# Kernel optimization log

Measured on AMD Instinct MI355X. Metric: run time of the kernel, lower is better.

## Reference

```python
import jax, jax.numpy as jnp
import numpy as np

ALPHA = 1.702  # sigmoid-GLU scale
LIMIT = 7.0    # clamp limit
TOP_K = 2      # num_experts_per_tok


def setup_inputs() -> dict:
    key = jax.random.key(0)
    ks = jax.random.split(key, 4)
    B, S, H, E, I = 2, 1024, 1024, 8, 2048
    return {
        "hidden_states": jax.random.normal(ks[0], (B, S, H), jnp.float32),
        "router_weight": jax.random.normal(ks[1], (E, H), jnp.float32),
        "router_bias": jnp.zeros((E,), jnp.float32),
        "gate_up_proj": jax.random.normal(ks[2], (E, H, 2 * I), jnp.float32) * 0.02,
        "gate_up_bias": jnp.zeros((E, 2 * I), jnp.float32),
        "down_proj": jax.random.normal(ks[3], (E, I, H), jnp.float32) * 0.02,
        "down_bias": jnp.zeros((E, H), jnp.float32),
    }


def reference(hidden_states, router_weight, router_bias, gate_up_proj,
              gate_up_bias, down_proj, down_bias):
    B, S, H = hidden_states.shape
    E, _, two_I = gate_up_proj.shape
    I = two_I // 2

    flat = hidden_states.reshape(B * S, H)  # [T, H]

    # Router: softmax + top-k
    logits = flat @ router_weight.T + router_bias            # [T, E]
    scores = jax.nn.softmax(logits, axis=-1)
    topk_w, topk_idx = jax.lax.top_k(scores, TOP_K)          # [T, K]

    # Dense per-expert gated FFN (einsum 'abmh,ehn->abemn' computes all experts
    # on all tokens; the reshape/permute dance is a mathematical no-op).
    gu = jnp.einsum('th,ehn->ten', flat, gate_up_proj) + gate_up_bias  # [T, E, 2I]
    gate = jnp.minimum(gu[..., :I], LIMIT)
    up = jnp.clip(gu[..., I:], -LIMIT, LIMIT)
    glu = gate * jax.nn.sigmoid(gate * ALPHA)
    act = (up + 1.0) * glu                                   # [T, E, I]

    down = jnp.einsum('tei,eih->teh', act, down_proj) + down_bias  # [T, E, H]

    # Combine: gather each token's top-k expert outputs, weighted sum.
    gathered = jnp.take_along_axis(down, topk_idx[:, :, None], axis=1)  # [T, K, H]
    out = (gathered * topk_w[:, :, None]).sum(axis=1)        # [T, H]
    return out.reshape(B, S, H)
```

## Files before the change

### kernel.cpp

```cpp
#include <hip/hip_runtime.h>
#include <math.h>

#define TT 2048
#define HH 1024
#define EE 8
#define II 2048
#define N1 4096
#define ALPHA 1.702f
#define LIMIT 7.0f

typedef __attribute__((ext_vector_type(8))) short short8;
typedef __attribute__((ext_vector_type(4))) float floatx4;
typedef __attribute__((ext_vector_type(4))) unsigned int uintx4;

__device__ __forceinline__ short f2bf(float f) {
  union { float f; unsigned u; } v; v.f = f;
  unsigned r = (v.u + 0x7fffu + ((v.u >> 16) & 1u)) >> 16;
  return (short)r;
}
__device__ __forceinline__ unsigned cvt2(float lo, float hi) {
  unsigned r;
  asm("v_cvt_pk_bf16_f32 %0, %1, %2" : "=v"(r) : "v"(lo), "v"(hi));
  return r;
}
__device__ __forceinline__ void gload16(const void* g, void* l) {
  __builtin_amdgcn_global_load_lds(
      (const __attribute__((address_space(1))) unsigned int*)g,
      (__attribute__((address_space(3))) unsigned int*)l, 16, 0, 0);
}

__global__ __launch_bounds__(256) void convert_x(const float* __restrict__ x,
                                                 unsigned short* __restrict__ xb) {
  const int id = blockIdx.x * 256 + threadIdx.x;
  const float4 a = ((const float4*)x)[id * 2];
  const float4 b = ((const float4*)x)[id * 2 + 1];
  uintx4 w;
  w[0] = cvt2(a.x, a.y); w[1] = cvt2(a.z, a.w);
  w[2] = cvt2(b.x, b.y); w[3] = cvt2(b.z, b.w);
  ((uintx4*)xb)[id] = w;
}

__global__ __launch_bounds__(256) void transpose_bf16(
    const float* __restrict__ src, unsigned short* __restrict__ dst,
    const int K, const int N) {
  const int e = blockIdx.z;
  const int n0 = blockIdx.x * 64, k0 = blockIdx.y * 64;
  __shared__ float tile[64][68];
  const float* s = src + (size_t)e * K * N;
  unsigned short* d = dst + (size_t)e * N * K;
  const int t = threadIdx.x;
  const int nq = t & 15, kr = t >> 4;
#pragma unroll
  for (int r = 0; r < 4; r++) {
    const int k = r * 16 + kr;
    const float4 v = *(const float4*)(s + (size_t)(k0 + k) * N + n0 + nq * 4);
    tile[k][nq * 4 + 0] = v.x; tile[k][nq * 4 + 1] = v.y;
    tile[k][nq * 4 + 2] = v.z; tile[k][nq * 4 + 3] = v.w;
  }
  __syncthreads();
  const int n = t >> 2, ks = (t & 3) * 16;
  unsigned short* orow = d + (size_t)(n0 + n) * K + k0 + ks;
  uintx4 w0, w1;
#pragma unroll
  for (int m = 0; m < 4; m++)
    w0[m] = cvt2(tile[ks + 2 * m][n], tile[ks + 2 * m + 1][n]);
#pragma unroll
  for (int m = 0; m < 4; m++)
    w1[m] = cvt2(tile[ks + 8 + 2 * m][n], tile[ks + 9 + 2 * m][n]);
  *(uintx4*)orow = w0;
  *(uintx4*)(orow + 8) = w1;
}

__global__ __launch_bounds__(256) void router_kernel(
    const float* __restrict__ x, const float* __restrict__ rw,
    const float* __restrict__ rb, int* __restrict__ topk_idx,
    float* __restrict__ topk_w) {
  const int t = blockIdx.x;
  const float* xr = x + (size_t)t * HH;
  const int lane = threadIdx.x & 63;
  const int wave = threadIdx.x >> 6;
  float xv[16];
#pragma unroll
  for (int i = 0; i < 16; i++) xv[i] = xr[lane + i * 64];
  __shared__ float logits[EE];
#pragma unroll
  for (int ee = 0; ee < 2; ee++) {
    const int e = wave * 2 + ee;
    const float* wr = rw + (size_t)e * HH;
    float s = 0.f;
#pragma unroll
    for (int i = 0; i < 16; i++) s += xv[i] * wr[lane + i * 64];
#pragma unroll
    for (int off = 32; off > 0; off >>= 1) s += __shfl_down(s, off, 64);
    if (lane == 0) logits[e] = s + rb[e];
  }
  __syncthreads();
  if (threadIdx.x == 0) {
    float l[EE], sc[EE];
    float mx = -3.4e38f;
    for (int i = 0; i < EE; i++) { l[i] = logits[i]; mx = fmaxf(mx, l[i]); }
    float sum = 0.f;
    for (int i = 0; i < EE; i++) { sc[i] = expf(l[i] - mx); sum += sc[i]; }
    const float inv = 1.f / sum;
    int i0 = 0;
    for (int i = 1; i < EE; i++) if (sc[i] > sc[i0]) i0 = i;
    int i1 = (i0 == 0) ? 1 : 0;
    for (int i = 0; i < EE; i++) if (i != i0 && sc[i] > sc[i1]) i1 = i;
    topk_idx[t * 2 + 0] = i0;
    topk_idx[t * 2 + 1] = i1;
    topk_w[t * 2 + 0] = sc[i0] * inv;
    topk_w[t * 2 + 1] = sc[i1] * inv;
  }
}

__global__ void assign_kernel(const int* __restrict__ topk_idx,
                              int* __restrict__ counts, int* __restrict__ rows) {
  const int id = blockIdx.x * blockDim.x + threadIdx.x;
  if (id >= TT * 2) return;
  const int e = topk_idx[id];
  const int slot = atomicAdd(&counts[e], 1);
  rows[e * TT + slot] = id;
}

__global__ __launch_bounds__(256, 4) void gemm_gu(
    const unsigned short* __restrict__ xb, const unsigned short* __restrict__ gupt,
    const float* __restrict__ gub, const int* __restrict__ counts,
    const int* __restrict__ rows, unsigned short* __restrict__ act) {
  const int e = blockIdx.z, mtile = blockIdx.y, ntile = blockIdx.x;
  const int count = counts[e];
  if (mtile * 128 >= count) return;
  const int* rl = rows + e * TT + mtile * 128;
  __shared__ __align__(16) char smem[33280];
  unsigned short* As = (unsigned short*)smem;
  unsigned short* Bs = (unsigned short*)(smem + 16384);
  float* glds = (float*)smem;
  const int tid = threadIdx.x;
  const int lane = tid & 63, wave = tid >> 6;
  const int wm = (wave & 1) << 6, wn = (wave >> 1) << 6;
  const int quad = lane >> 4, r16 = lane & 15;

  const int lrow = lane >> 2, lko = (lane & 3) * 8;
  const int q0 = wave * 2, q1 = q0 + 1;
  const int row0 = q0 * 16 + lrow, row1 = q1 * 16 + lrow;
  const int last = count - 1 - mtile * 128;
  const int cr0 = row0 <= last ? row0 : last;
  const int cr1 = row1 <= last ? row1 : last;
  const unsigned short* pA0 = xb + (size_t)(rl[cr0] >> 1) * HH + lko;
  const unsigned short* pA1 = xb + (size_t)(rl[cr1] >> 1) * HH + lko;
  const int bn0 = (row0 < 64) ? (ntile * 64 + row0) : (II + ntile * 64 + row0 - 64);
  const int bn1 = (row1 < 64) ? (ntile * 64 + row1) : (II + ntile * 64 + row1 - 64);
  const unsigned short* pB0 = gupt + (size_t)e * N1 * HH + (size_t)bn0 * HH + lko;
  const unsigned short* pB1 = gupt + (size_t)e * N1 * HH + (size_t)bn1 * HH + lko;
  unsigned short* dA0 = As + q0 * 512;
  unsigned short* dA1 = As + q1 * 512;
  unsigned short* dB0 = Bs + q0 * 512;
  unsigned short* dB1 = Bs + q1 * 512;

  floatx4 acc[4][4] = {};
  const int NTK = HH / 32;

#define STAGE(B, kk) do { \
    const int ko_ = (kk) * 32; \
    gload16(pA0 + ko_, dA0 + (B) * 4096); \
    gload16(pA1 + ko_, dA1 + (B) * 4096); \
    gload16(pB0 + ko_, dB0 + (B) * 4096); \
    gload16(pB1 + ko_, dB1 + (B) * 4096); \
  } while (0)

#define PHASE(B) do { \
    asm volatile("s_waitcnt vmcnt(4)" ::: "memory"); \
    __builtin_amdgcn_s_barrier(); \
    short8 af[4], bf4[4]; \
    _Pragma("unroll") for (int i = 0; i < 4; i++) \
      af[i] = *(const short8*)(As + (B) * 4096 + (wm + i * 16 + r16) * 32 + quad * 8); \
    _Pragma("unroll") for (int j = 0; j < 4; j++) \
      bf4[j] = *(const short8*)(Bs + (B) * 4096 + (wn + j * 16 + r16) * 32 + quad * 8); \
    asm volatile("s_waitcnt lgkmcnt(0)" ::: "memory"); \
    __builtin_amdgcn_sched_barrier(0); \
    __builtin_amdgcn_s_barrier(); \
    { const int ks_ = kn < NTK ? kn : NTK - 1; kn++; STAGE(B, ks_); } \
    __builtin_amdgcn_sched_barrier(0); \
    __builtin_amdgcn_s_setprio(1); \
    _Pragma("unroll") for (int i = 0; i < 4; i++) \
      _Pragma("unroll") for (int j = 0; j < 4; j++) \
        acc[i][j] = __builtin_amdgcn_mfma_f32_16x16x32_bf16(af[i], bf4[j], acc[i][j], 0, 0, 0); \
    __builtin_amdgcn_s_setprio(0); \
  } while (0)

  STAGE(0, 0);
  STAGE(1, 1);
  int kn = 2;
#pragma unroll 1
  for (int t = 0; t < NTK; t += 2) {
    PHASE(0);
    PHASE(1);
  }
  asm volatile("s_waitcnt vmcnt(0)" ::: "memory");
  __builtin_amdgcn_s_barrier();

  const int colbase = ntile * 64;
  if (wn == 0) {
#pragma unroll
    for (int j = 0; j < 4; j++) {
      const int c = j * 16 + r16;
      const float gb = gub[e * N1 + colbase + c];
#pragma unroll
      for (int i = 0; i < 4; i++)
#pragma unroll
        for (int reg = 0; reg < 4; reg++) {
          const int rr = wm + i * 16 + quad * 4 + reg;
          float g = acc[i][j][reg] + gb;
          g = fminf(g, LIMIT);
          glds[rr * 65 + c] = g / (1.f + expf(-g * ALPHA));
        }
    }
  }
  __builtin_amdgcn_s_barrier();
  if (wn == 64) {
#pragma unroll
    for (int j = 0; j < 4; j++) {
      const int c = j * 16 + r16;
      const float ub = gub[e * N1 + II + colbase + c];
#pragma unroll
      for (int i = 0; i < 4; i++)
#pragma unroll
        for (int reg = 0; reg < 4; reg++) {
          const int rr = wm + i * 16 + quad * 4 + reg;
          if (mtile * 128 + rr < count) {
            float u = acc[i][j][reg] + ub;
            u = fminf(fmaxf(u, -LIMIT), LIMIT);
            const float glu = glds[rr * 65 + c];
            act[(size_t)rl[rr] * II + colbase + c] = (unsigned short)f2bf((u + 1.f) * glu);
          }
        }
    }
  }
#undef STAGE
#undef PHASE
}

__global__ __launch_bounds__(256, 4) void gemm_down(
    const unsigned short* __restrict__ act, const unsigned short* __restrict__ dpt,
    const float* __restrict__ db, const int* __restrict__ counts,
    const int* __restrict__ rows, float* __restrict__ dout) {
  const int e = blockIdx.z >> 2, kc = blockIdx.z & 3;
  const int mtile = blockIdx.y, ntile = blockIdx.x;
  const int count = counts[e];
  if (mtile * 128 >= count) return;
  const int kb = kc * (II / 4);
  const int* rl = rows + e * TT + mtile * 128;
  __shared__ __align__(16) char smem[32768];
  unsigned short* As = (unsigned short*)smem;
  unsigned short* Bs = (unsigned short*)(smem + 16384);
  const int tid = threadIdx.x;
  const int lane = tid & 63, wave = tid >> 6;
  const int wm = (wave & 1) << 6, wn = (wave >> 1) << 6;
  const int quad = lane >> 4, r16 = lane & 15;

  const int lrow = lane >> 2, lko = (lane & 3) * 8;
  const int q0 = wave * 2, q1 = q0 + 1;
  const int row0 = q0 * 16 + lrow, row1 = q1 * 16 + lrow;
  const int last = count - 1 - mtile * 128;
  const int cr0 = row0 <= last ? row0 : last;
  const int cr1 = row1 <= last ? row1 : last;
  const unsigned short* pA0 = act + (size_t)rl[cr0] * II + kb + lko;
  const unsigned short* pA1 = act + (size_t)rl[cr1] * II + kb + lko;
  const unsigned short* pB0 = dpt + (size_t)e * HH * II + (size_t)(ntile * 128 + row0) * II + kb + lko;
  const unsigned short* pB1 = dpt + (size_t)e * HH * II + (size_t)(ntile * 128 + row1) * II + kb + lko;
  unsigned short* dA0 = As + q0 * 512;
  unsigned short* dA1 = As + q1 * 512;
  unsigned short* dB0 = Bs + q0 * 512;
  unsigned short* dB1 = Bs + q1 * 512;

  floatx4 acc[4][4] = {};
  const int NTK = (II / 4) / 32;

#define STAGE(B, kk) do { \
    const int ko_ = (kk) * 32; \
    gload16(pA0 + ko_, dA0 + (B) * 4096); \
    gload16(pA1 + ko_, dA1 + (B) * 4096); \
    gload16(pB0 + ko_, dB0 + (B) * 4096); \
    gload16(pB1 + ko_, dB1 + (B) * 4096); \
  } while (0)

#define PHASE(B) do { \
    asm volatile("s_waitcnt vmcnt(4)" ::: "memory"); \
    __builtin_amdgcn_s_barrier(); \
    short8 af[4], bf4[4]; \
    _Pragma("unroll") for (int i = 0; i < 4; i++) \
      af[i] = *(const short8*)(As + (B) * 4096 + (wm + i * 16 + r16) * 32 + quad * 8); \
    _Pragma("unroll") for (int j = 0; j < 4; j++) \
      bf4[j] = *(const short8*)(Bs + (B) * 4096 + (wn + j * 16 + r16) * 32 + quad * 8); \
    asm volatile("s_waitcnt lgkmcnt(0)" ::: "memory"); \
    __builtin_amdgcn_sched_barrier(0); \
    __builtin_amdgcn_s_barrier(); \
    { const int ks_ = kn < NTK ? kn : NTK - 1; kn++; STAGE(B, ks_); } \
    __builtin_amdgcn_sched_barrier(0); \
    __builtin_amdgcn_s_setprio(1); \
    _Pragma("unroll") for (int i = 0; i < 4; i++) \
      _Pragma("unroll") for (int j = 0; j < 4; j++) \
        acc[i][j] = __builtin_amdgcn_mfma_f32_16x16x32_bf16(af[i], bf4[j], acc[i][j], 0, 0, 0); \
    __builtin_amdgcn_s_setprio(0); \
  } while (0)

  STAGE(0, 0);
  STAGE(1, 1);
  int kn = 2;
#pragma unroll 1
  for (int t = 0; t < NTK; t += 2) {
    PHASE(0);
    PHASE(1);
  }
  asm volatile("s_waitcnt vmcnt(0)" ::: "memory");
  __builtin_amdgcn_s_barrier();

  float* dc = dout + (size_t)kc * ((size_t)TT * 2 * HH);
#pragma unroll
  for (int i = 0; i < 4; i++) {
#pragma unroll
    for (int reg = 0; reg < 4; reg++) {
      const int rr = wm + i * 16 + quad * 4 + reg;
      if (mtile * 128 + rr < count) {
        const int ent = rl[rr];
        float* orow = dc + (size_t)ent * HH + ntile * 128;
#pragma unroll
        for (int j = 0; j < 4; j++) {
          const int c = wn + j * 16 + r16;
          float v = acc[i][j][reg];
          if (kc == 0) v += db[e * HH + ntile * 128 + c];
          orow[c] = v;
        }
      }
    }
  }
#undef STAGE
#undef PHASE
}

__global__ void combine_kernel(const float* __restrict__ dout,
                               const float* __restrict__ tw,
                               float* __restrict__ out) {
  const int id = blockIdx.x * blockDim.x + threadIdx.x;
  const int t = id >> 8;
  const int h = (id & 255) * 4;
  const float w0 = tw[t * 2], w1 = tw[t * 2 + 1];
  const size_t CH = (size_t)TT * 2 * HH;
  const size_t r0 = (size_t)(2 * t) * HH + h;
  const size_t r1 = (size_t)(2 * t + 1) * HH + h;
  float4 a = {0.f, 0.f, 0.f, 0.f}, b = {0.f, 0.f, 0.f, 0.f};
#pragma unroll
  for (int c = 0; c < 4; c++) {
    const float4 va = *(const float4*)(dout + c * CH + r0);
    const float4 vb = *(const float4*)(dout + c * CH + r1);
    a.x += va.x; a.y += va.y; a.z += va.z; a.w += va.w;
    b.x += vb.x; b.y += vb.y; b.z += vb.z; b.w += vb.w;
  }
  float4 o;
  o.x = w0 * a.x + w1 * b.x;
  o.y = w0 * a.y + w1 * b.y;
  o.z = w0 * a.z + w1 * b.z;
  o.w = w0 * a.w + w1 * b.w;
  *(float4*)(out + (size_t)t * HH + h) = o;
}

extern "C" void kernel_launch(void* const* d_in, const int* in_sizes, int n_in,
                              void* d_out, int out_size, void* d_ws, size_t ws_size,
                              hipStream_t stream) {
  const float* x   = (const float*)d_in[0];
  const float* rw  = (const float*)d_in[1];
  const float* rb  = (const float*)d_in[2];
  const float* gup = (const float*)d_in[3];
  const float* gub = (const float*)d_in[4];
  const float* dp  = (const float*)d_in[5];
  const float* db  = (const float*)d_in[6];
  float* out = (float*)d_out;

  char* ws = (char*)d_ws;
  int*   topk_idx = (int*)(ws + 0);
  float* topk_w   = (float*)(ws + 16384);
  int*   counts   = (int*)(ws + 32768);
  int*   rows     = (int*)(ws + 33024);
  unsigned short* xb   = (unsigned short*)(ws + 131072);
  unsigned short* gupt = (unsigned short*)(ws + 4325376);
  unsigned short* dpt  = (unsigned short*)(ws + 71434240);
  unsigned short* act  = (unsigned short*)(ws + 104988672);
  float* dout = (float*)(ws + 4325376);

  convert_x<<<TT * HH / 8 / 256, 256, 0, stream>>>(x, xb);
  transpose_bf16<<<dim3(N1 / 64, HH / 64, EE), 256, 0, stream>>>(gup, gupt, HH, N1);
  transpose_bf16<<<dim3(HH / 64, II / 64, EE), 256, 0, stream>>>(dp, dpt, II, HH);
  router_kernel<<<TT, 256, 0, stream>>>(x, rw, rb, topk_idx, topk_w);
  hipMemsetAsync(counts, 0, 64, stream);
  assign_kernel<<<(TT * 2 + 255) / 256, 256, 0, stream>>>(topk_idx, counts, rows);
  gemm_gu<<<dim3(II / 64, TT / 128, EE), 256, 0, stream>>>(xb, gupt, gub, counts, rows, act);
  gemm_down<<<dim3(HH / 128, TT / 128, EE * 4), 256, 0, stream>>>(act, dpt, db, counts, rows, dout);
  combine_kernel<<<(TT * HH / 4) / 256, 256, 0, stream>>>(dout, topk_w, out);
}
```

Measured before the change: 429.1 us.

## Fuse router with bf16 conversion and assignment, combine via atomics, deepen pipeline

Folds the x-to-bf16 conversion and the expert-slot assignment into the router kernel, which removes two launches. The combine kernel and the partial-sum buffer go away: the down GEMM now scales by the top-k weight and atomically adds into a zeroed output, with the K split cut from 4 to 2. Both GEMMs move from a 2-stage to a 4-stage LDS pipeline with 64KB shared memory and launch bounds lowered to 2 blocks. The trade-offs are fewer resident blocks per CU, float atomic contention on the output, and a nondeterministic order of accumulation.

```diff
diff --git a/kernel.cpp b/kernel.cpp
--- a/kernel.cpp
+++ b/kernel.cpp
@@ -27,17 +27,6 @@
   __builtin_amdgcn_global_load_lds(
       (const __attribute__((address_space(1))) unsigned int*)g,
       (__attribute__((address_space(3))) unsigned int*)l, 16, 0, 0);
-}
-
-__global__ __launch_bounds__(256) void convert_x(const float* __restrict__ x,
-                                                 unsigned short* __restrict__ xb) {
-  const int id = blockIdx.x * 256 + threadIdx.x;
-  const float4 a = ((const float4*)x)[id * 2];
-  const float4 b = ((const float4*)x)[id * 2 + 1];
-  uintx4 w;
-  w[0] = cvt2(a.x, a.y); w[1] = cvt2(a.z, a.w);
-  w[2] = cvt2(b.x, b.y); w[3] = cvt2(b.z, b.w);
-  ((uintx4*)xb)[id] = w;
 }
 
 __global__ __launch_bounds__(256) void transpose_bf16(
@@ -73,8 +62,9 @@
 
 __global__ __launch_bounds__(256) void router_kernel(
     const float* __restrict__ x, const float* __restrict__ rw,
-    const float* __restrict__ rb, int* __restrict__ topk_idx,
-    float* __restrict__ topk_w) {
+    const float* __restrict__ rb, float* __restrict__ topk_w,
+    int* __restrict__ counts, int* __restrict__ rows,
+    unsigned short* __restrict__ xb) {
   const int t = blockIdx.x;
   const float* xr = x + (size_t)t * HH;
   const int lane = threadIdx.x & 63;
@@ -93,6 +83,11 @@
 #pragma unroll
     for (int off = 32; off > 0; off >>= 1) s += __shfl_down(s, off, 64);
     if (lane == 0) logits[e] = s + rb[e];
+  }
+  if (wave == 0) {
+    unsigned short* xo = xb + (size_t)t * HH;
+#pragma unroll
+    for (int i = 0; i < 16; i++) xo[lane + i * 64] = (unsigned short)f2bf(xv[i]);
   }
   __syncthreads();
   if (threadIdx.x == 0) {
@@ -106,23 +101,16 @@
     for (int i = 1; i < EE; i++) if (sc[i] > sc[i0]) i0 = i;
     int i1 = (i0 == 0) ? 1 : 0;
     for (int i = 0; i < EE; i++) if (i != i0 && sc[i] > sc[i1]) i1 = i;
-    topk_idx[t * 2 + 0] = i0;
-    topk_idx[t * 2 + 1] = i1;
     topk_w[t * 2 + 0] = sc[i0] * inv;
     topk_w[t * 2 + 1] = sc[i1] * inv;
-  }
-}
-
-__global__ void assign_kernel(const int* __restrict__ topk_idx,
-                              int* __restrict__ counts, int* __restrict__ rows) {
-  const int id = blockIdx.x * blockDim.x + threadIdx.x;
-  if (id >= TT * 2) return;
-  const int e = topk_idx[id];
-  const int slot = atomicAdd(&counts[e], 1);
-  rows[e * TT + slot] = id;
-}
-
-__global__ __launch_bounds__(256, 4) void gemm_gu(
+    const int s0 = atomicAdd(&counts[i0], 1);
+    rows[i0 * TT + s0] = t * 2 + 0;
+    const int s1 = atomicAdd(&counts[i1], 1);
+    rows[i1 * TT + s1] = t * 2 + 1;
+  }
+}
+
+__global__ __launch_bounds__(256, 2) void gemm_gu(
     const unsigned short* __restrict__ xb, const unsigned short* __restrict__ gupt,
     const float* __restrict__ gub, const int* __restrict__ counts,
     const int* __restrict__ rows, unsigned short* __restrict__ act) {
@@ -130,9 +118,9 @@
   const int count = counts[e];
   if (mtile * 128 >= count) return;
   const int* rl = rows + e * TT + mtile * 128;
-  __shared__ __align__(16) char smem[33280];
+  __shared__ __align__(16) char smem[65536];
   unsigned short* As = (unsigned short*)smem;
-  unsigned short* Bs = (unsigned short*)(smem + 16384);
+  unsigned short* Bs = (unsigned short*)(smem + 32768);
   float* glds = (float*)smem;
   const int tid = threadIdx.x;
   const int lane = tid & 63, wave = tid >> 6;
@@ -168,7 +156,7 @@
   } while (0)
 
 #define PHASE(B) do { \
-    asm volatile("s_waitcnt vmcnt(4)" ::: "memory"); \
+    asm volatile("s_waitcnt vmcnt(12)" ::: "memory"); \
     __builtin_amdgcn_s_barrier(); \
     short8 af[4], bf4[4]; \
     _Pragma("unroll") for (int i = 0; i < 4; i++) \
@@ -189,11 +177,15 @@
 
   STAGE(0, 0);
   STAGE(1, 1);
-  int kn = 2;
+  STAGE(2, 2);
+  STAGE(3, 3);
+  int kn = 4;
 #pragma unroll 1
-  for (int t = 0; t < NTK; t += 2) {
+  for (int t = 0; t < NTK; t += 4) {
     PHASE(0);
     PHASE(1);
+    PHASE(2);
+    PHASE(3);
   }
   asm volatile("s_waitcnt vmcnt(0)" ::: "memory");
   __builtin_amdgcn_s_barrier();
@@ -239,19 +231,20 @@
 #undef PHASE
 }
 
-__global__ __launch_bounds__(256, 4) void gemm_down(
+__global__ __launch_bounds__(256, 2) void gemm_down(
     const unsigned short* __restrict__ act, const unsigned short* __restrict__ dpt,
     const float* __restrict__ db, const int* __restrict__ counts,
-    const int* __restrict__ rows, float* __restrict__ dout) {
-  const int e = blockIdx.z >> 2, kc = blockIdx.z & 3;
+    const int* __restrict__ rows, const float* __restrict__ tw,
+    float* __restrict__ out) {
+  const int e = blockIdx.z >> 1, kc = blockIdx.z & 1;
   const int mtile = blockIdx.y, ntile = blockIdx.x;
   const int count = counts[e];
   if (mtile * 128 >= count) return;
-  const int kb = kc * (II / 4);
+  const int kb = kc * (II / 2);
   const int* rl = rows + e * TT + mtile * 128;
-  __shared__ __align__(16) char smem[32768];
+  __shared__ __align__(16) char smem[65536];
   unsigned short* As = (unsigned short*)smem;
-  unsigned short* Bs = (unsigned short*)(smem + 16384);
+  unsigned short* Bs = (unsigned short*)(smem + 32768);
   const int tid = threadIdx.x;
   const int lane = tid & 63, wave = tid >> 6;
   const int wm = (wave & 1) << 6, wn = (wave >> 1) << 6;
@@ -273,7 +266,7 @@
   unsigned short* dB1 = Bs + q1 * 512;
 
   floatx4 acc[4][4] = {};
-  const int NTK = (II / 4) / 32;
+  const int NTK = (II / 2) / 32;
 
 #define STAGE(B, kk) do { \
     const int ko_ = (kk) * 32; \
@@ -284,7 +277,7 @@
   } while (0)
 
 #define PHASE(B) do { \
-    asm volatile("s_waitcnt vmcnt(4)" ::: "memory"); \
+    asm volatile("s_waitcnt vmcnt(12)" ::: "memory"); \
     __builtin_amdgcn_s_barrier(); \
     short8 af[4], bf4[4]; \
     _Pragma("unroll") for (int i = 0; i < 4; i++) \
@@ -305,16 +298,19 @@
 
   STAGE(0, 0);
   STAGE(1, 1);
-  int kn = 2;
+  STAGE(2, 2);
+  STAGE(3, 3);
+  int kn = 4;
 #pragma unroll 1
-  for (int t = 0; t < NTK; t += 2) {
+  for (int t = 0; t < NTK; t += 4) {
     PHASE(0);
     PHASE(1);
+    PHASE(2);
+    PHASE(3);
   }
   asm volatile("s_waitcnt vmcnt(0)" ::: "memory");
   __builtin_amdgcn_s_barrier();
 
-  float* dc = dout + (size_t)kc * ((size_t)TT * 2 * HH);
 #pragma unroll
   for (int i = 0; i < 4; i++) {
 #pragma unroll
@@ -322,45 +318,20 @@
       const int rr = wm + i * 16 + quad * 4 + reg;
       if (mtile * 128 + rr < count) {
         const int ent = rl[rr];
-        float* orow = dc + (size_t)ent * HH + ntile * 128;
+        const float w = tw[ent];
+        float* orow = out + (size_t)(ent >> 1) * HH + ntile * 128;
 #pragma unroll
         for (int j = 0; j < 4; j++) {
           const int c = wn + j * 16 + r16;
           float v = acc[i][j][reg];
           if (kc == 0) v += db[e * HH + ntile * 128 + c];
-          orow[c] = v;
+          atomicAdd(&orow[c], w * v);
         }
       }
     }
   }
 #undef STAGE
 #undef PHASE
-}
-
-__global__ void combine_kernel(const float* __restrict__ dout,
-                               const float* __restrict__ tw,
-                               float* __restrict__ out) {
-  const int id = blockIdx.x * blockDim.x + threadIdx.x;
-  const int t = id >> 8;
-  const int h = (id & 255) * 4;
-  const float w0 = tw[t * 2], w1 = tw[t * 2 + 1];
-  const size_t CH = (size_t)TT * 2 * HH;
-  const size_t r0 = (size_t)(2 * t) * HH + h;
-  const size_t r1 = (size_t)(2 * t + 1) * HH + h;
-  float4 a = {0.f, 0.f, 0.f, 0.f}, b = {0.f, 0.f, 0.f, 0.f};
-#pragma unroll
-  for (int c = 0; c < 4; c++) {
-    const float4 va = *(const float4*)(dout + c * CH + r0);
-    const float4 vb = *(const float4*)(dout + c * CH + r1);
-    a.x += va.x; a.y += va.y; a.z += va.z; a.w += va.w;
-    b.x += vb.x; b.y += vb.y; b.z += vb.z; b.w += vb.w;
-  }
-  float4 o;
-  o.x = w0 * a.x + w1 * b.x;
-  o.y = w0 * a.y + w1 * b.y;
-  o.z = w0 * a.z + w1 * b.z;
-  o.w = w0 * a.w + w1 * b.w;
-  *(float4*)(out + (size_t)t * HH + h) = o;
 }
 
 extern "C" void kernel_launch(void* const* d_in, const int* in_sizes, int n_in,
@@ -376,23 +347,19 @@
   float* out = (float*)d_out;
 
   char* ws = (char*)d_ws;
-  int*   topk_idx = (int*)(ws + 0);
-  float* topk_w   = (float*)(ws + 16384);
-  int*   counts   = (int*)(ws + 32768);
-  int*   rows     = (int*)(ws + 33024);
+  float* topk_w   = (float*)(ws + 0);
+  int*   counts   = (int*)(ws + 16384);
+  int*   rows     = (int*)(ws + 16640);
   unsigned short* xb   = (unsigned short*)(ws + 131072);
   unsigned short* gupt = (unsigned short*)(ws + 4325376);
   unsigned short* dpt  = (unsigned short*)(ws + 71434240);
   unsigned short* act  = (unsigned short*)(ws + 104988672);
-  float* dout = (float*)(ws + 4325376);
-
-  convert_x<<<TT * HH / 8 / 256, 256, 0, stream>>>(x, xb);
+
+  hipMemsetAsync(counts, 0, 64, stream);
+  hipMemsetAsync(out, 0, (size_t)TT * HH * 4, stream);
+  router_kernel<<<TT, 256, 0, stream>>>(x, rw, rb, topk_w, counts, rows, xb);
   transpose_bf16<<<dim3(N1 / 64, HH / 64, EE), 256, 0, stream>>>(gup, gupt, HH, N1);
   transpose_bf16<<<dim3(HH / 64, II / 64, EE), 256, 0, stream>>>(dp, dpt, II, HH);
-  router_kernel<<<TT, 256, 0, stream>>>(x, rw, rb, topk_idx, topk_w);
-  hipMemsetAsync(counts, 0, 64, stream);
-  assign_kernel<<<(TT * 2 + 255) / 256, 256, 0, stream>>>(topk_idx, counts, rows);
   gemm_gu<<<dim3(II / 64, TT / 128, EE), 256, 0, stream>>>(xb, gupt, gub, counts, rows, act);
-  gemm_down<<<dim3(HH / 128, TT / 128, EE * 4), 256, 0, stream>>>(act, dpt, db, counts, rows, dout);
-  combine_kernel<<<(TT * HH / 4) / 256, 256, 0, stream>>>(dout, topk_w, out);
-}
+  gemm_down<<<dim3(HH / 128, TT / 128, EE * 2), 256, 0, stream>>>(act, dpt, db, counts, rows, topk_w, out);
+}
```

After: 484.1 us. 12.8% more time.
